# Performance work log

Measured on AMD Instinct MI355X. Metric: run time of the kernel, lower is better.

## Reference

```python
import jax, jax.numpy as jnp
import numpy as np

N, E, B = 25000, 400000, 64
IN, HID, OUT, EDGE, TDIM, L = 16, 128, 16, 16, 64, 4
EIN = 2 * HID + 1 + EDGE  # 273


def _sinusoidal(t, dim):
    half = dim // 2
    freqs = jnp.exp(jnp.arange(half, dtype=jnp.float32) * (-np.log(10000.0) / (half - 1)))
    a = t[:, None] * freqs[None, :]
    return jnp.concatenate([jnp.sin(a), jnp.cos(a)], axis=-1)


def _layernorm(h, g, b, eps=1e-5):
    mu = h.mean(-1, keepdims=True)
    v = h.var(-1, keepdims=True)
    return (h - mu) / jnp.sqrt(v + eps) * g + b


def setup_inputs() -> dict:
    key = jax.random.key(0)
    ks = iter(jax.random.split(key, 64))

    def rn(shape, scale=0.05):
        return jax.random.normal(next(ks), shape, dtype=jnp.float32) * scale

    inp = {
        'h': jax.random.normal(next(ks), (N, IN), dtype=jnp.float32),
        'x': jax.random.normal(next(ks), (N, 3), dtype=jnp.float32),
        'edge_index': jax.random.randint(next(ks), (2, E), 0, N),
        't': jax.random.uniform(next(ks), (B,), dtype=jnp.float32) * 1000.0,
        'edge_attr': jax.random.normal(next(ks), (E, EDGE), dtype=jnp.float32),
        'batch': jnp.sort(jax.random.randint(next(ks), (N,), 0, B)),
        # embeddings
        'node_w': rn((IN, HID)), 'node_b': jnp.zeros((HID,), jnp.float32),
        'tw1': rn((TDIM, HID)), 'tb1': jnp.zeros((HID,), jnp.float32),
        'tw2': rn((HID, HID)), 'tb2': jnp.zeros((HID,), jnp.float32),
        # per-layer stacked params (L, ...)
        'edge_w1': rn((L, EIN, HID)), 'edge_b1': jnp.zeros((L, HID), jnp.float32),
        'edge_w2': rn((L, HID, HID)), 'edge_b2': jnp.zeros((L, HID), jnp.float32),
        'att_w': rn((L, HID, 1)), 'att_b': jnp.zeros((L, 1), jnp.float32),
        'cw1': rn((L, HID, HID)), 'cb1': jnp.zeros((L, HID), jnp.float32),
        'cw2': rn((L, HID, 1), scale=0.001),  # xavier gain=0.001
        'nw1': rn((L, 2 * HID, HID)), 'nb1': jnp.zeros((L, HID), jnp.float32),
        'nw2': rn((L, HID, HID)), 'nb2': jnp.zeros((L, HID), jnp.float32),
        'ln_g': jnp.ones((L, HID), jnp.float32), 'ln_b': jnp.zeros((L, HID), jnp.float32),
        # heads
        'out_w1': rn((HID, HID)), 'out_b1': jnp.zeros((HID,), jnp.float32),
        'out_w2': rn((HID, OUT)), 'out_b2': jnp.zeros((OUT,), jnp.float32),
        'head_w': rn((HID, 3), scale=0.01), 'head_b': jnp.zeros((3,), jnp.float32),
    }
    return inp


def reference(h, x, edge_index, t, edge_attr, batch,
              node_w, node_b, tw1, tb1, tw2, tb2,
              edge_w1, edge_b1, edge_w2, edge_b2, att_w, att_b,
              cw1, cb1, cw2, nw1, nb1, nw2, nb2, ln_g, ln_b,
              out_w1, out_b1, out_w2, out_b2, head_w, head_b):
    silu = jax.nn.silu
    n_nodes = h.shape[0]
    row, col = edge_index[0], edge_index[1]

    # node + time embedding
    h = h @ node_w + node_b
    te = _sinusoidal(t, TDIM)
    te = silu(te @ tw1 + tb1) @ tw2 + tb2
    h = h + te[batch]

    for i in range(L):
        coord_diff = x[row] - x[col]                      # (E, 3)
        radial = (coord_diff ** 2).sum(-1, keepdims=True)  # (E, 1)
        edge_in = jnp.concatenate([h[row], h[col], radial, edge_attr], axis=-1)
        m = silu(silu(edge_in @ edge_w1[i] + edge_b1[i]) @ edge_w2[i] + edge_b2[i])
        att = jax.nn.sigmoid(m @ att_w[i] + att_b[i])
        m = m * att
        cw = silu(m @ cw1[i] + cb1[i]) @ cw2[i]           # (E, 1)
        coord_diff = coord_diff / jnp.sqrt(radial + 1e-8)  # normalize=True
        x = x + jax.ops.segment_sum(coord_diff * cw, row, num_segments=n_nodes)
        m_i = jax.ops.segment_sum(m, row, num_segments=n_nodes)
        h_in = jnp.concatenate([h, m_i], axis=-1)
        h_new = h + (silu(h_in @ nw1[i] + nb1[i]) @ nw2[i] + nb2[i])
        h = _layernorm(h_new, ln_g[i], ln_b[i])

    h_out = silu(h @ out_w1 + out_b1) @ out_w2 + out_b2  # (N, OUT)
    x_out = h @ head_w + head_b                           # (N, 3)
    return h_out, x_out
```

## Files before the change

kernel.cpp:

```cpp
#include <hip/hip_runtime.h>
#include <hip/hip_bf16.h>
#include <cmath>

#define NN      25000
#define NEDGE   400000
#define NBATCH  64
#define IN_DIM  16
#define HID     128
#define OUT_DIM 16
#define EDGE_DIM 16
#define TDIM    64
#define NL      4
#define EIN     273
#define EPB     64
#define W2KB    16
#define A_PAD   65
#define A3OFF   (16*A_PAD*8)
#define NPB     32
#define NPAD    33

typedef short bfrag __attribute__((ext_vector_type(8)));
typedef float ffrag __attribute__((ext_vector_type(4)));

__device__ __forceinline__ float siluf(float v) { return v / (1.f + __expf(-v)); }
__device__ __forceinline__ float sigm(float v)  { return 1.f / (1.f + __expf(-v)); }
__device__ __forceinline__ unsigned short f2b(float f) {
    unsigned u = __float_as_uint(f);
    u = (u + 0x7FFFu + ((u >> 16) & 1u)) >> 16;
    return (unsigned short)u;
}
__device__ __forceinline__ float b2f(unsigned short b) {
    return __uint_as_float(((unsigned)b) << 16);
}
__device__ __forceinline__ int ileave(int n) {
    return (n & 0x60) | ((n & 15) << 1) | ((n >> 4) & 1);
}

__global__ __launch_bounds__(256) void hist_kernel(const int* __restrict__ row, int* __restrict__ deg) {
    const int tid = blockIdx.x * 256 + threadIdx.x;
    if (tid < NEDGE) atomicAdd(&deg[row[tid]], 1);
}

__global__ __launch_bounds__(1024) void scan_kernel(const int* __restrict__ deg, int* __restrict__ row_start) {
    __shared__ int part[1024];
    const int tid = threadIdx.x;
    const int base = tid * 25;
    int sum = 0;
    for (int i = 0; i < 25; i++) { const int idx = base + i; if (idx < NN) sum += deg[idx]; }
    part[tid] = sum;
    __syncthreads();
    for (int off = 1; off < 1024; off <<= 1) {
        int v = (tid >= off) ? part[tid - off] : 0;
        __syncthreads();
        part[tid] += v;
        __syncthreads();
    }
    int run = part[tid] - sum;
    for (int i = 0; i < 25; i++) {
        const int idx = base + i;
        if (idx < NN) { row_start[idx] = run; run += deg[idx]; }
    }
    if (tid == 1023) row_start[NN] = part[1023];
}

__global__ __launch_bounds__(256) void scatter_kernel(
    const int* __restrict__ row, const int* __restrict__ col,
    const int* __restrict__ row_start, int* __restrict__ cursor,
    int* __restrict__ rowp, int* __restrict__ colp, int* __restrict__ eorder)
{
    const int tid = blockIdx.x * 256 + threadIdx.x;
    if (tid >= NEDGE) return;
    const int r = row[tid];
    const int pos = row_start[r] + atomicAdd(&cursor[r], 1);
    rowp[pos] = r; colp[pos] = col[tid]; eorder[pos] = tid;
}

__global__ __launch_bounds__(256) void ea_pack(
    const float* __restrict__ ea, const int* __restrict__ eorder, unsigned short* __restrict__ eabp)
{
    const int tid = blockIdx.x * 256 + threadIdx.x;
    if (tid >= NEDGE) return;
    const int e = eorder[tid];
    const float4* src = (const float4*)&ea[(size_t)e * 16];
    bfrag o0, o1;
    #pragma unroll
    for (int q = 0; q < 2; q++) {
        const float4 a = src[q];
        o0[q*4+0] = (short)f2b(a.x); o0[q*4+1] = (short)f2b(a.y);
        o0[q*4+2] = (short)f2b(a.z); o0[q*4+3] = (short)f2b(a.w);
    }
    #pragma unroll
    for (int q = 0; q < 2; q++) {
        const float4 a = src[2+q];
        o1[q*4+0] = (short)f2b(a.x); o1[q*4+1] = (short)f2b(a.y);
        o1[q*4+2] = (short)f2b(a.z); o1[q*4+3] = (short)f2b(a.w);
    }
    *(bfrag*)&eabp[(size_t)tid * 16]     = o0;
    *(bfrag*)&eabp[(size_t)tid * 16 + 8] = o1;
}

__global__ __launch_bounds__(256) void prep_w(
    const float* __restrict__ ew1, const float* __restrict__ ew2, const float* __restrict__ cw1,
    unsigned short* __restrict__ w1x, unsigned short* __restrict__ w1rp,
    unsigned short* __restrict__ w1cp, unsigned short* __restrict__ w2p,
    unsigned short* __restrict__ c1p)
{
    const int PER_L = 68 * 128;
    int tid = blockIdx.x * 256 + threadIdx.x;
    if (tid >= NL * PER_L) return;
    const int l = tid / PER_L, rem = tid % PER_L;
    const int kb = rem >> 7, n = rem & 127;
    unsigned short o[8];
    const float* W1 = ew1 + (size_t)l * EIN * HID;
    if (kb < 4) {
        const int nc = ileave(n);
        #pragma unroll
        for (int j = 0; j < 8; j++) {
            const int kk = kb * 8 + j;
            const int ok = (kk < 16) ? (257 + kk) : (kk == 16 ? 256 : -1);
            o[j] = (ok >= 0) ? f2b(W1[(size_t)ok * HID + nc]) : (unsigned short)0;
        }
        #pragma unroll
        for (int j = 0; j < 8; j++) w1x[(((size_t)l * 4 + kb) * 128 + n) * 8 + j] = o[j];
    } else if (kb < 20) {
        const int kb2 = kb - 4;
        const int nc = ileave(n);
        #pragma unroll
        for (int j = 0; j < 8; j++) o[j] = f2b(W1[(size_t)(kb2 * 8 + j) * HID + nc]);
        #pragma unroll
        for (int j = 0; j < 8; j++) w1rp[(((size_t)l * 16 + kb2) * 128 + n) * 8 + j] = o[j];
    } else if (kb < 36) {
        const int kb2 = kb - 20;
        const int nc = ileave(n);
        #pragma unroll
        for (int j = 0; j < 8; j++) o[j] = f2b(W1[(size_t)(128 + kb2 * 8 + j) * HID + nc]);
        #pragma unroll
        for (int j = 0; j < 8; j++) w1cp[(((size_t)l * 16 + kb2) * 128 + n) * 8 + j] = o[j];
    } else if (kb < 52) {
        const int kb2 = kb - 36;
        const float* W = ew2 + (size_t)l * HID * HID;
        const int nc = ileave(n);
        #pragma unroll
        for (int j = 0; j < 8; j++) o[j] = f2b(W[(size_t)(kb2 * 8 + j) * HID + nc]);
        #pragma unroll
        for (int j = 0; j < 8; j++) w2p[(((size_t)l * W2KB + kb2) * 128 + n) * 8 + j] = o[j];
    } else {
        const int kb2 = kb - 52;
        const float* W = cw1 + (size_t)l * HID * HID;
        #pragma unroll
        for (int j = 0; j < 8; j++) o[j] = f2b(W[(size_t)(kb2 * 8 + j) * HID + n]);
        #pragma unroll
        for (int j = 0; j < 8; j++) c1p[(((size_t)l * W2KB + kb2) * 128 + n) * 8 + j] = o[j];
    }
}

__global__ __launch_bounds__(256) void prep_w2(
    const float* __restrict__ nw1, const float* __restrict__ nw2,
    const float* __restrict__ ow1, const float* __restrict__ ow2,
    unsigned short* __restrict__ n1p, unsigned short* __restrict__ n2p,
    unsigned short* __restrict__ o1p, unsigned short* __restrict__ o2p)
{
    const int C1 = NL * 32 * 128;
    const int C2 = C1 + NL * 16 * 128;
    const int C3 = C2 + 16 * 128;
    const int C4 = C3 + 16 * 16;
    int tid = blockIdx.x * 256 + threadIdx.x;
    if (tid >= C4) return;
    if (tid < C1) {
        const int l = tid / (32*128), rem = tid % (32*128);
        const int kb = rem >> 7, n = rem & 127;
        const int nc = ileave(n);
        #pragma unroll
        for (int j = 0; j < 8; j++)
            n1p[(size_t)tid*8 + j] = f2b(nw1[((size_t)l*256 + kb*8 + j)*128 + nc]);
    } else if (tid < C2) {
        const int t2 = tid - C1;
        const int l = t2 / (16*128), rem = t2 % (16*128);
        const int kb = rem >> 7, n = rem & 127;
        const int nc = ileave(n);
        #pragma unroll
        for (int j = 0; j < 8; j++)
            n2p[(size_t)t2*8 + j] = f2b(nw2[((size_t)l*128 + kb*8 + j)*128 + nc]);
    } else if (tid < C3) {
        const int t2 = tid - C2;
        const int kb = t2 >> 7, n = t2 & 127;
        #pragma unroll
        for (int j = 0; j < 8; j++)
            o1p[(size_t)t2*8 + j] = f2b(ow1[(size_t)(kb*8 + j)*128 + n]);
    } else {
        const int t2 = tid - C3;
        const int kb = t2 >> 4, n = t2 & 15;
        #pragma unroll
        for (int j = 0; j < 8; j++)
            o2p[(size_t)t2*8 + j] = f2b(ow2[(size_t)(kb*8 + j)*16 + n]);
    }
}

__global__ __launch_bounds__(HID) void te_kernel(
    const float* __restrict__ t, const float* __restrict__ tw1, const float* __restrict__ tb1,
    const float* __restrict__ tw2, const float* __restrict__ tb2, float* __restrict__ te_out)
{
    __shared__ float s0[TDIM];
    __shared__ float s1[HID];
    const int b = blockIdx.x, j = threadIdx.x;
    const float tv = t[b];
    if (j < TDIM) {
        const int k = j & 31;
        const float freq = expf((float)k * (-logf(10000.f) / 31.f));
        const float a = tv * freq;
        s0[j] = (j < 32) ? sinf(a) : cosf(a);
    }
    __syncthreads();
    float acc = tb1[j];
    for (int k = 0; k < TDIM; k++) acc += s0[k] * tw1[k*HID + j];
    s1[j] = siluf(acc);
    __syncthreads();
    float acc2 = tb2[j];
    for (int k = 0; k < HID; k++) acc2 += s1[k] * tw2[k*HID + j];
    te_out[b*HID + j] = acc2;
}

__global__ __launch_bounds__(256) void embed_kernel(
    const float* __restrict__ h_in, const float* __restrict__ x_in,
    const int* __restrict__ batch,
    const float* __restrict__ node_w, const float* __restrict__ node_b,
    const float* __restrict__ te, float* __restrict__ h, unsigned short* __restrict__ hbf,
    float* __restrict__ x0, float* __restrict__ m_i)
{
    __shared__ float hs[2][IN_DIM];
    const int local = threadIdx.x >> 7;
    const int j = threadIdx.x & 127;
    const int n = blockIdx.x * 2 + local;
    if (j < IN_DIM) hs[local][j] = h_in[n*IN_DIM + j];
    if (j >= 64 && j < 67) x0[n*3 + (j - 64)] = x_in[n*3 + (j - 64)];
    __syncthreads();
    float acc = node_b[j];
    #pragma unroll
    for (int k = 0; k < IN_DIM; k++) acc += hs[local][k] * node_w[k*HID + j];
    acc += te[batch[n]*HID + j];
    h[(size_t)n*HID + j]   = acc;
    hbf[(size_t)n*HID + j] = f2b(acc);
    m_i[(size_t)n*HID + j] = 0.f;
}

__global__ __launch_bounds__(256) void pq_kernel(
    const unsigned short* __restrict__ hbf,
    const unsigned short* __restrict__ Wr, const unsigned short* __restrict__ Wc,
    unsigned short* __restrict__ P, unsigned short* __restrict__ Q)
{
    __shared__ unsigned short sA[16 * A_PAD * 8];
    const int t = threadIdx.x, lane = t & 63, w = t >> 6;
    const int quad = lane >> 4, colid = lane & 15;
    const int n0 = blockIdx.x * 64;

    #pragma unroll
    for (int it = 0; it < 4; it++) {
        const int c = t + it * 256;
        const int e = c >> 4, kb = c & 15;
        const int nidx = min(n0 + e, NN - 1);
        *(bfrag*)&sA[(kb*A_PAD + e) * 8] = *(const bfrag*)&hbf[(size_t)nidx * HID + kb * 8];
    }
    __syncthreads();

    ffrag aP[4][2] = {}, aQ[4][2] = {};
    for (int ks = 0; ks < 4; ks++) {
        const int kb = ks * 4 + quad;
        const bfrag p0 = *(const bfrag*)&Wr[((size_t)kb * 128 + w*32 + colid) * 8];
        const bfrag p1 = *(const bfrag*)&Wr[((size_t)kb * 128 + w*32 + 16 + colid) * 8];
        const bfrag q0 = *(const bfrag*)&Wc[((size_t)kb * 128 + w*32 + colid) * 8];
        const bfrag q1 = *(const bfrag*)&Wc[((size_t)kb * 128 + w*32 + 16 + colid) * 8];
        #pragma unroll
        for (int mt = 0; mt < 4; mt++) {
            const bfrag a = *(const bfrag*)&sA[(kb*A_PAD + mt*16 + colid) * 8];
            aP[mt][0] = __builtin_amdgcn_mfma_f32_16x16x32_bf16(a, p0, aP[mt][0], 0, 0, 0);
            aP[mt][1] = __builtin_amdgcn_mfma_f32_16x16x32_bf16(a, p1, aP[mt][1], 0, 0, 0);
            aQ[mt][0] = __builtin_amdgcn_mfma_f32_16x16x32_bf16(a, q0, aQ[mt][0], 0, 0, 0);
            aQ[mt][1] = __builtin_amdgcn_mfma_f32_16x16x32_bf16(a, q1, aQ[mt][1], 0, 0, 0);
        }
    }
    const int f0 = w*32 + 2*colid;
    #pragma unroll
    for (int mt = 0; mt < 4; mt++)
        #pragma unroll
        for (int reg = 0; reg < 4; reg++) {
            const int n = n0 + mt*16 + quad*4 + reg;
            if (n < NN) {
                *(__hip_bfloat162*)&P[(size_t)n*HID + f0] =
                    __float22bfloat162_rn(make_float2(aP[mt][0][reg], aP[mt][1][reg]));
                *(__hip_bfloat162*)&Q[(size_t)n*HID + f0] =
                    __float22bfloat162_rn(make_float2(aQ[mt][0][reg], aQ[mt][1][reg]));
            }
        }
}

__global__ __launch_bounds__(256) void edge_mfma(
    const unsigned short* __restrict__ P, const unsigned short* __restrict__ Q,
    const float* __restrict__ x,
    float* __restrict__ x_new, float* __restrict__ m_i,
    const int* __restrict__ rowp, const int* __restrict__ colp,
    const unsigned short* __restrict__ eabp,
    const unsigned short* __restrict__ W1X, const float* __restrict__ B1,
    const unsigned short* __restrict__ W2p, const float* __restrict__ B2,
    const unsigned short* __restrict__ C1p, const float* __restrict__ CB1,
    const float* __restrict__ AW, const float* __restrict__ ABv,
    const float* __restrict__ CW2)
{
    __shared__ unsigned short sA[32 * A_PAD * 8];
    __shared__ int rc[EPB][2];
    __shared__ float AWs[HID];
    float* scr   = (float*)sA;
    float* attS  = scr;
    float* cpart = scr + 64;

    const int t = threadIdx.x;
    const int e0 = blockIdx.x * EPB;
    const int lane = t & 63, w = t >> 6;
    const int quad = lane >> 4, colid = lane & 15;
    const int f0 = w*32 + 2*colid;

    float cd0 = 0.f, cd1 = 0.f, cd2 = 0.f;
    if (t < EPB) {
        const int r = rowp[e0 + t], c = colp[e0 + t];
        rc[t][0] = r; rc[t][1] = c;
        const float dx = x[r*3+0] - x[c*3+0];
        const float dy = x[r*3+1] - x[c*3+1];
        const float dz = x[r*3+2] - x[c*3+2];
        const float rad = dx*dx + dy*dy + dz*dz;
        const float inv = 1.f / sqrtf(rad + 1e-8f);
        cd0 = dx*inv; cd1 = dy*inv; cd2 = dz*inv;
        unsigned short* p2 = &sA[A3OFF + (2*A_PAD + t) * 8];
        p2[0] = f2b(rad);
        #pragma unroll
        for (int j = 1; j < 8; j++) p2[j] = 0;
        unsigned short* p3 = &sA[A3OFF + (3*A_PAD + t) * 8];
        #pragma unroll
        for (int j = 0; j < 8; j++) p3[j] = 0;
    }
    if (t >= 128 && t < 256) AWs[t - 128] = AW[t - 128];
    if (t < 128) {
        const int e = t >> 1, hh = t & 1;
        *(bfrag*)&sA[A3OFF + (hh*A_PAD + e) * 8] = *(const bfrag*)&eabp[(size_t)(e0 + e) * 16 + hh * 8];
    }
    __syncthreads();

    ffrag accea[4][2];
    {
        const float b0v = B1[f0], b1v = B1[f0+1];
        #pragma unroll
        for (int mt = 0; mt < 4; mt++)
            #pragma unroll
            for (int r = 0; r < 4; r++) { accea[mt][0][r] = b0v; accea[mt][1][r] = b1v; }
    }
    {
        const bfrag eb0 = *(const bfrag*)&W1X[((size_t)quad * 128 + w*32 + colid) * 8];
        const bfrag eb1 = *(const bfrag*)&W1X[((size_t)quad * 128 + w*32 + 16 + colid) * 8];
        #pragma unroll
        for (int mt = 0; mt < 4; mt++) {
            const bfrag a = *(const bfrag*)&sA[A3OFF + (quad*A_PAD + mt*16 + colid) * 8];
            accea[mt][0] = __builtin_amdgcn_mfma_f32_16x16x32_bf16(a, eb0, accea[mt][0], 0, 0, 0);
            accea[mt][1] = __builtin_amdgcn_mfma_f32_16x16x32_bf16(a, eb1, accea[mt][1], 0, 0, 0);
        }
    }

    {
        const int kb = f0 >> 3, j = f0 & 7;
        #pragma unroll
        for (int mt = 0; mt < 4; mt++) {
            unsigned pv[4], qv[4];
            #pragma unroll
            for (int reg = 0; reg < 4; reg++) {
                const int e = mt*16 + quad*4 + reg;
                pv[reg] = *(const unsigned*)&P[(size_t)rc[e][0]*HID + f0];
                qv[reg] = *(const unsigned*)&Q[(size_t)rc[e][1]*HID + f0];
            }
            #pragma unroll
            for (int reg = 0; reg < 4; reg++) {
                const int e = mt*16 + quad*4 + reg;
                const float v0 = siluf(__uint_as_float(pv[reg] << 16)
                                     + __uint_as_float(qv[reg] << 16) + accea[mt][0][reg]);
                const float v1 = siluf(__uint_as_float(pv[reg] & 0xFFFF0000u)
                                     + __uint_as_float(qv[reg] & 0xFFFF0000u) + accea[mt][1][reg]);
                *(__hip_bfloat162*)&sA[(kb*A_PAD + e) * 8 + j] =
                    __float22bfloat162_rn(make_float2(v0, v1));
            }
        }
    }
    __syncthreads();

    ffrag acc2[4][2] = {};
    for (int ks = 0; ks < 4; ks++) {
        const int kb = ks * 4 + quad;
        const bfrag b0 = *(const bfrag*)&W2p[((size_t)kb * 128 + w*32 + colid) * 8];
        const bfrag b1 = *(const bfrag*)&W2p[((size_t)kb * 128 + w*32 + 16 + colid) * 8];
        #pragma unroll
        for (int mt = 0; mt < 4; mt++) {
            const bfrag a = *(const bfrag*)&sA[(kb*A_PAD + mt*16 + colid) * 8];
            acc2[mt][0] = __builtin_amdgcn_mfma_f32_16x16x32_bf16(a, b0, acc2[mt][0], 0, 0, 0);
            acc2[mt][1] = __builtin_amdgcn_mfma_f32_16x16x32_bf16(a, b1, acc2[mt][1], 0, 0, 0);
        }
    }
    {
        const int kb = f0 >> 3, j = f0 & 7;
        const float b0v = B2[f0], b1v = B2[f0+1];
        #pragma unroll
        for (int mt = 0; mt < 4; mt++)
            #pragma unroll
            for (int reg = 0; reg < 4; reg++) {
                const float v0 = siluf(acc2[mt][0][reg] + b0v);
                const float v1 = siluf(acc2[mt][1][reg] + b1v);
                const int e = mt*16 + quad*4 + reg;
                *(__hip_bfloat162*)&sA[A3OFF + (kb*A_PAD + e) * 8 + j] =
                    __float22bfloat162_rn(make_float2(v0, v1));
            }
    }
    __syncthreads();

    {
        const int e = t >> 2, q = t & 3;
        float s = 0.f;
        #pragma unroll
        for (int kk = 0; kk < 4; kk++) {
            const int kb = q*4 + kk;
            const bfrag v = *(const bfrag*)&sA[A3OFF + (kb*A_PAD + e) * 8];
            #pragma unroll
            for (int j = 0; j < 8; j++) s += b2f((unsigned short)v[j]) * AWs[kb*8 + j];
        }
        s += __shfl_xor(s, 1);
        s += __shfl_xor(s, 2);
        if (q == 0) attS[e] = sigm(s + ABv[0]);
    }
    __syncthreads();

    ffrag acc3[4][2] = {};
    for (int ks = 0; ks < 4; ks++) {
        const int kb = ks * 4 + quad;
        const bfrag b0 = *(const bfrag*)&C1p[((size_t)kb * 128 + w*32 + colid) * 8];
        const bfrag b1 = *(const bfrag*)&C1p[((size_t)kb * 128 + w*32 + 16 + colid) * 8];
        #pragma unroll
        for (int mt = 0; mt < 4; mt++) {
            const bfrag a = *(const bfrag*)&sA[A3OFF + (kb*A_PAD + mt*16 + colid) * 8];
            acc3[mt][0] = __builtin_amdgcn_mfma_f32_16x16x32_bf16(a, b0, acc3[mt][0], 0, 0, 0);
            acc3[mt][1] = __builtin_amdgcn_mfma_f32_16x16x32_bf16(a, b1, acc3[mt][1], 0, 0, 0);
        }
    }

    {
        const int fkb0 = lane >> 3,     fj = lane & 7;
        const int fkb1 = 8 + (lane >> 3);
        float a0 = 0.f, a1 = 0.f;
        for (int i = 0; i < 16; i++) {
            const int e = (w << 4) + i;
            const float av = attS[e];
            const int r = rc[e][0];
            a0 += b2f(sA[A3OFF + (fkb0*A_PAD + e) * 8 + fj]) * av;
            a1 += b2f(sA[A3OFF + (fkb1*A_PAD + e) * 8 + fj]) * av;
            const bool flush = (i == 15) || (rc[e+1][0] != r);
            if (flush) {
                atomicAdd(&m_i[(size_t)r * HID + lane],      a0);
                atomicAdd(&m_i[(size_t)r * HID + lane + 64], a1);
                a0 = 0.f; a1 = 0.f;
            }
        }
    }

    {
        const float cb0v = CB1[w*32 + colid], cb1v = CB1[w*32 + 16 + colid];
        const float cwv0 = CW2[w*32 + colid], cwv1 = CW2[w*32 + 16 + colid];
        float att_r[4][4];
        #pragma unroll
        for (int mt = 0; mt < 4; mt++) {
            const float4 a4 = *(const float4*)&attS[mt*16 + quad*4];
            att_r[mt][0] = a4.x; att_r[mt][1] = a4.y; att_r[mt][2] = a4.z; att_r[mt][3] = a4.w;
        }
        float p[4][4];
        #pragma unroll
        for (int mt = 0; mt < 4; mt++)
            #pragma unroll
            for (int reg = 0; reg < 4; reg++)
                p[mt][reg] = siluf(att_r[mt][reg] * acc3[mt][0][reg] + cb0v) * cwv0
                           + siluf(att_r[mt][reg] * acc3[mt][1][reg] + cb1v) * cwv1;
        __syncthreads();
        #pragma unroll
        for (int mt = 0; mt < 4; mt++)
            #pragma unroll
            for (int reg = 0; reg < 4; reg++) {
                float s = p[mt][reg];
                s += __shfl_xor(s, 1);
                s += __shfl_xor(s, 2);
                s += __shfl_xor(s, 4);
                s += __shfl_xor(s, 8);
                if (colid == 0) cpart[(mt*16 + quad*4 + reg) * 4 + w] = s;
            }
    }
    __syncthreads();
    if (t < EPB) {
        const float s = cpart[t*4+0] + cpart[t*4+1] + cpart[t*4+2] + cpart[t*4+3];
        const int r = rc[t][0];
        atomicAdd(&x_new[r*3+0], cd0 * s);
        atomicAdd(&x_new[r*3+1], cd1 * s);
        atomicAdd(&x_new[r*3+2], cd2 * s);
    }
}

__global__ __launch_bounds__(256) void node_mfma(
    float* __restrict__ h, unsigned short* __restrict__ hbf, float* __restrict__ m_i,
    const unsigned short* __restrict__ N1p, const float* __restrict__ NB1,
    const unsigned short* __restrict__ N2p, const float* __restrict__ NB2,
    const float* __restrict__ LG, const float* __restrict__ LB)
{
    __shared__ unsigned short sA[32 * NPAD * 8];
    __shared__ float mu_s[NPB], rs_s[NPB];
    float* hres = (float*)sA;

    const int t = threadIdx.x, lane = t & 63, w = t >> 6;
    const int quad = lane >> 4, colid = lane & 15;
    const int n0 = blockIdx.x * NPB;

    #pragma unroll
    for (int it = 0; it < 2; it++) {
        const int c = t + it * 256;
        const int e = c >> 4, kb = c & 15;
        const int nidx = min(n0 + e, NN - 1);
        *(bfrag*)&sA[(kb*NPAD + e) * 8] = *(const bfrag*)&hbf[(size_t)nidx * HID + kb * 8];
    }
    #pragma unroll
    for (int it = 0; it < 2; it++) {
        const int c = t + it * 256;
        const int e = c >> 4, kb = c & 15;
        const int nidx = min(n0 + e, NN - 1);
        const float4 v0 = *(const float4*)&m_i[(size_t)nidx * HID + kb * 8];
        const float4 v1 = *(const float4*)&m_i[(size_t)nidx * HID + kb * 8 + 4];
        bfrag bv;
        bv[0]=(short)f2b(v0.x); bv[1]=(short)f2b(v0.y); bv[2]=(short)f2b(v0.z); bv[3]=(short)f2b(v0.w);
        bv[4]=(short)f2b(v1.x); bv[5]=(short)f2b(v1.y); bv[6]=(short)f2b(v1.z); bv[7]=(short)f2b(v1.w);
        *(bfrag*)&sA[((16 + kb)*NPAD + e) * 8] = bv;
        if (n0 + e < NN) {
            const float4 z4 = {0.f, 0.f, 0.f, 0.f};
            *(float4*)&m_i[(size_t)nidx * HID + kb * 8]     = z4;
            *(float4*)&m_i[(size_t)nidx * HID + kb * 8 + 4] = z4;
        }
    }
    __syncthreads();

    const int f0 = w*32 + 2*colid;
    ffrag acc1[2][2];
    {
        const float b0v = NB1[f0], b1v = NB1[f0+1];
        #pragma unroll
        for (int mt = 0; mt < 2; mt++)
            #pragma unroll
            for (int r = 0; r < 4; r++) { acc1[mt][0][r] = b0v; acc1[mt][1][r] = b1v; }
    }
    for (int ks = 0; ks < 8; ks++) {
        const int kb = ks * 4 + quad;
        const bfrag b0 = *(const bfrag*)&N1p[((size_t)kb * 128 + w*32 + colid) * 8];
        const bfrag b1 = *(const bfrag*)&N1p[((size_t)kb * 128 + w*32 + 16 + colid) * 8];
        #pragma unroll
        for (int mt = 0; mt < 2; mt++) {
            const bfrag a = *(const bfrag*)&sA[(kb*NPAD + mt*16 + colid) * 8];
            acc1[mt][0] = __builtin_amdgcn_mfma_f32_16x16x32_bf16(a, b0, acc1[mt][0], 0, 0, 0);
            acc1[mt][1] = __builtin_amdgcn_mfma_f32_16x16x32_bf16(a, b1, acc1[mt][1], 0, 0, 0);
        }
    }
    __syncthreads();
    {
        const int kb = f0 >> 3, j = f0 & 7;
        #pragma unroll
        for (int mt = 0; mt < 2; mt++)
            #pragma unroll
            for (int reg = 0; reg < 4; reg++) {
                const float v0 = siluf(acc1[mt][0][reg]);
                const float v1 = siluf(acc1[mt][1][reg]);
                const int e = mt*16 + quad*4 + reg;
                *(__hip_bfloat162*)&sA[(kb*NPAD + e) * 8 + j] =
                    __float22bfloat162_rn(make_float2(v0, v1));
            }
    }
    __syncthreads();

    ffrag acc2[2][2];
    {
        const float b0v = NB2[f0], b1v = NB2[f0+1];
        #pragma unroll
        for (int mt = 0; mt < 2; mt++)
            #pragma unroll
            for (int r = 0; r < 4; r++) { acc2[mt][0][r] = b0v; acc2[mt][1][r] = b1v; }
    }
    for (int ks = 0; ks < 4; ks++) {
        const int kb = ks * 4 + quad;
        const bfrag b0 = *(const bfrag*)&N2p[((size_t)kb * 128 + w*32 + colid) * 8];
        const bfrag b1 = *(const bfrag*)&N2p[((size_t)kb * 128 + w*32 + 16 + colid) * 8];
        #pragma unroll
        for (int mt = 0; mt < 2; mt++) {
            const bfrag a = *(const bfrag*)&sA[(kb*NPAD + mt*16 + colid) * 8];
            acc2[mt][0] = __builtin_amdgcn_mfma_f32_16x16x32_bf16(a, b0, acc2[mt][0], 0, 0, 0);
            acc2[mt][1] = __builtin_amdgcn_mfma_f32_16x16x32_bf16(a, b1, acc2[mt][1], 0, 0, 0);
        }
    }
    __syncthreads();
    {
        #pragma unroll
        for (int mt = 0; mt < 2; mt++)
            #pragma unroll
            for (int reg = 0; reg < 4; reg++) {
                const int row = mt*16 + quad*4 + reg;
                const int nidx = min(n0 + row, NN - 1);
                const float2 hr = *(const float2*)&h[(size_t)nidx*HID + f0];
                float2 o;
                o.x = acc2[mt][0][reg] + hr.x;
                o.y = acc2[mt][1][reg] + hr.y;
                *(float2*)&hres[row*130 + f0] = o;
            }
    }
    __syncthreads();
    {
        const int row = t >> 3, q = t & 7;
        float s = 0.f, s2 = 0.f;
        #pragma unroll
        for (int i = 0; i < 16; i++) {
            const float v = hres[row*130 + q*16 + i];
            s += v; s2 += v*v;
        }
        s += __shfl_xor(s, 1); s2 += __shfl_xor(s2, 1);
        s += __shfl_xor(s, 2); s2 += __shfl_xor(s2, 2);
        s += __shfl_xor(s, 4); s2 += __shfl_xor(s2, 4);
        if (q == 0) {
            const float mu = s * (1.f/HID);
            mu_s[row] = mu;
            rs_s[row] = rsqrtf(s2 * (1.f/HID) - mu*mu + 1e-5f);
        }
    }
    __syncthreads();
    for (int idx = t; idx < NPB*HID; idx += 256) {
        const int row = idx >> 7, f = idx & 127;
        const int n = n0 + row;
        if (n < NN) {
            const float v = (hres[row*130 + f] - mu_s[row]) * rs_s[row] * LG[f] + LB[f];
            h[(size_t)n*HID + f]   = v;
            hbf[(size_t)n*HID + f] = f2b(v);
        }
    }
}

__global__ __launch_bounds__(256) void out_mfma(
    const unsigned short* __restrict__ hbf,
    const unsigned short* __restrict__ O1p, const float* __restrict__ OB1,
    const unsigned short* __restrict__ O2p, const float* __restrict__ OB2,
    const float* __restrict__ HW, const float* __restrict__ HB,
    float* __restrict__ out)
{
    __shared__ unsigned short sA[32 * A_PAD * 8];
    __shared__ float hws[HID*3];
    const int A2O = 16 * A_PAD * 8;

    const int t = threadIdx.x, lane = t & 63, w = t >> 6;
    const int quad = lane >> 4, colid = lane & 15;
    const int n0 = blockIdx.x * 64;

    if (t < 128)      { hws[t] = HW[t]; hws[t+128] = HW[t+128]; }
    else if (t < 256) { const int i = t - 128 + 256; if (i < 384) hws[i] = HW[i]; }
    #pragma unroll
    for (int it = 0; it < 4; it++) {
        const int c = t + it * 256;
        const int e = c >> 4, kb = c & 15;
        const int nidx = min(n0 + e, NN - 1);
        *(bfrag*)&sA[(kb*A_PAD + e) * 8] = *(const bfrag*)&hbf[(size_t)nidx * HID + kb * 8];
    }
    __syncthreads();

    ffrag acc1[4][2];
    {
        const float b0v = OB1[w*32 + colid], b1v = OB1[w*32 + 16 + colid];
        #pragma unroll
        for (int mt = 0; mt < 4; mt++)
            #pragma unroll
            for (int r = 0; r < 4; r++) { acc1[mt][0][r] = b0v; acc1[mt][1][r] = b1v; }
    }
    for (int ks = 0; ks < 4; ks++) {
        const int kb = ks * 4 + quad;
        const bfrag b0 = *(const bfrag*)&O1p[((size_t)kb * 128 + w*32 + colid) * 8];
        const bfrag b1 = *(const bfrag*)&O1p[((size_t)kb * 128 + w*32 + 16 + colid) * 8];
        #pragma unroll
        for (int mt = 0; mt < 4; mt++) {
            const bfrag a = *(const bfrag*)&sA[(kb*A_PAD + mt*16 + colid) * 8];
            acc1[mt][0] = __builtin_amdgcn_mfma_f32_16x16x32_bf16(a, b0, acc1[mt][0], 0, 0, 0);
            acc1[mt][1] = __builtin_amdgcn_mfma_f32_16x16x32_bf16(a, b1, acc1[mt][1], 0, 0, 0);
        }
    }
    {
        #pragma unroll
        for (int mt = 0; mt < 4; mt++)
            #pragma unroll
            for (int nt = 0; nt < 2; nt++) {
                const int f = w*32 + nt*16 + colid;
                const int kb = f >> 3, j = f & 7;
                #pragma unroll
                for (int reg = 0; reg < 4; reg++) {
                    const float v = siluf(acc1[mt][nt][reg]);
                    const int e = mt*16 + quad*4 + reg;
                    sA[A2O + (kb*A_PAD + e) * 8 + j] = f2b(v);
                }
            }
    }
    __syncthreads();

    ffrag acco;
    {
        const float ob2v = OB2[colid];
        #pragma unroll
        for (int r = 0; r < 4; r++) acco[r] = ob2v;
    }
    for (int ks = 0; ks < 4; ks++) {
        const int kb = ks * 4 + quad;
        const bfrag a = *(const bfrag*)&sA[A2O + (kb*A_PAD + w*16 + colid) * 8];
        const bfrag b = *(const bfrag*)&O2p[((size_t)kb * 16 + colid) * 8];
        acco = __builtin_amdgcn_mfma_f32_16x16x32_bf16(a, b, acco, 0, 0, 0);
    }
    #pragma unroll
    for (int reg = 0; reg < 4; reg++) {
        const int rowg = w*16 + quad*4 + reg;
        const int n = n0 + rowg;
        if (n < NN) out[(size_t)n*OUT_DIM + colid] = acco[reg];
    }

    {
        const int rloc = t >> 2, q = t & 3;
        float s0 = 0.f, s1 = 0.f, s2 = 0.f;
        #pragma unroll
        for (int kk = 0; kk < 4; kk++) {
            const int kb = q*4 + kk;
            const bfrag v = *(const bfrag*)&sA[(kb*A_PAD + rloc) * 8];
            #pragma unroll
            for (int j = 0; j < 8; j++) {
                const float hv = b2f((unsigned short)v[j]);
                const int k = kb*8 + j;
                s0 += hv * hws[k*3+0]; s1 += hv * hws[k*3+1]; s2 += hv * hws[k*3+2];
            }
        }
        s0 += __shfl_xor(s0, 1); s1 += __shfl_xor(s1, 1); s2 += __shfl_xor(s2, 1);
        s0 += __shfl_xor(s0, 2); s1 += __shfl_xor(s1, 2); s2 += __shfl_xor(s2, 2);
        const int n = n0 + rloc;
        if (q == 0 && n < NN) {
            out[(size_t)NN*OUT_DIM + n*3 + 0] = s0 + HB[0];
            out[(size_t)NN*OUT_DIM + n*3 + 1] = s1 + HB[1];
            out[(size_t)NN*OUT_DIM + n*3 + 2] = s2 + HB[2];
        }
    }
}

extern "C" void kernel_launch(void* const* d_in, const int* in_sizes, int n_in,
                              void* d_out, int out_size, void* d_ws, size_t ws_size,
                              hipStream_t stream) {
    (void)in_sizes; (void)n_in; (void)out_size; (void)ws_size;
    const float* h_in      = (const float*)d_in[0];
    const float* x_in      = (const float*)d_in[1];
    const int*   edge_idx  = (const int*)  d_in[2];
    const float* t         = (const float*)d_in[3];
    const float* edge_attr = (const float*)d_in[4];
    const int*   batch     = (const int*)  d_in[5];
    const float* node_w = (const float*)d_in[6];
    const float* node_b = (const float*)d_in[7];
    const float* tw1    = (const float*)d_in[8];
    const float* tb1    = (const float*)d_in[9];
    const float* tw2    = (const float*)d_in[10];
    const float* tb2    = (const float*)d_in[11];
    const float* ew1    = (const float*)d_in[12];
    const float* eb1    = (const float*)d_in[13];
    const float* ew2    = (const float*)d_in[14];
    const float* eb2    = (const float*)d_in[15];
    const float* attw   = (const float*)d_in[16];
    const float* attb   = (const float*)d_in[17];
    const float* cw1    = (const float*)d_in[18];
    const float* cb1    = (const float*)d_in[19];
    const float* cw2    = (const float*)d_in[20];
    const float* nw1    = (const float*)d_in[21];
    const float* nb1    = (const float*)d_in[22];
    const float* nw2    = (const float*)d_in[23];
    const float* nb2    = (const float*)d_in[24];
    const float* lng    = (const float*)d_in[25];
    const float* lnb    = (const float*)d_in[26];
    const float* ow1    = (const float*)d_in[27];
    const float* ob1    = (const float*)d_in[28];
    const float* ow2    = (const float*)d_in[29];
    const float* ob2    = (const float*)d_in[30];
    const float* hw     = (const float*)d_in[31];
    const float* hb     = (const float*)d_in[32];

    const int* row = edge_idx;
    const int* col = edge_idx + NEDGE;

    float* ws  = (float*)d_ws;
    float* te  = ws;
    float* h   = te  + NBATCH*HID;
    float* m_i = h   + (size_t)NN*HID;
    float* x0  = m_i + (size_t)NN*HID;
    float* x1  = x0  + NN*3;
    unsigned short* hbf  = (unsigned short*)(x1 + NN*3);
    unsigned short* eabp = hbf + (size_t)NN*HID;
    unsigned short* w1x  = eabp + (size_t)NEDGE*EDGE_DIM;
    unsigned short* w1rp = w1x  + (size_t)NL*4*128*8;
    unsigned short* w1cp = w1rp + (size_t)NL*16*128*8;
    unsigned short* w2p  = w1cp + (size_t)NL*16*128*8;
    unsigned short* c1p  = w2p  + (size_t)NL*16*128*8;
    unsigned short* n1p  = c1p  + (size_t)NL*16*128*8;
    unsigned short* n2p  = n1p  + (size_t)NL*32*128*8;
    unsigned short* o1p  = n2p  + (size_t)NL*16*128*8;
    unsigned short* o2p  = o1p  + (size_t)16*128*8;
    unsigned short* Pq   = o2p  + (size_t)16*16*8;
    unsigned short* Qq   = Pq   + (size_t)NN*HID;
    int* deg       = (int*)(Qq + (size_t)NN*HID);
    int* row_start = deg + NN;
    int* cursor    = row_start + NN + 1;
    int* rowp      = cursor + NN;
    int* colp      = rowp + NEDGE;
    int* eorder    = colp + NEDGE;

    hipMemsetAsync(deg, 0, NN*sizeof(int), stream);
    hipMemsetAsync(cursor, 0, NN*sizeof(int), stream);
    hist_kernel<<<(NEDGE+255)/256, 256, 0, stream>>>(row, deg);
    scan_kernel<<<1, 1024, 0, stream>>>(deg, row_start);
    scatter_kernel<<<(NEDGE+255)/256, 256, 0, stream>>>(row, col, row_start, cursor, rowp, colp, eorder);
    ea_pack<<<(NEDGE+255)/256, 256, 0, stream>>>(edge_attr, eorder, eabp);

    prep_w<<<(NL*68*128 + 255)/256, 256, 0, stream>>>(ew1, ew2, cw1, w1x, w1rp, w1cp, w2p, c1p);
    prep_w2<<<(NL*32*128 + NL*16*128 + 16*128 + 16*16 + 255)/256, 256, 0, stream>>>(
        nw1, nw2, ow1, ow2, n1p, n2p, o1p, o2p);
    te_kernel<<<NBATCH, HID, 0, stream>>>(t, tw1, tb1, tw2, tb2, te);
    embed_kernel<<<NN/2, 256, 0, stream>>>(h_in, x_in, batch, node_w, node_b, te, h, hbf, x0, m_i);

    const int NBLK = (NN + NPB - 1) / NPB;
    const int OBLK = (NN + 63) / 64;
    float* xc = x0; float* xn = x1;
    for (int i = 0; i < NL; i++) {
        pq_kernel<<<OBLK, 256, 0, stream>>>(
            hbf, w1rp + (size_t)i*16*128*8, w1cp + (size_t)i*16*128*8, Pq, Qq);
        hipMemcpyAsync(xn, xc, (size_t)NN*3*sizeof(float), hipMemcpyDeviceToDevice, stream);
        edge_mfma<<<NEDGE/EPB, 256, 0, stream>>>(
            Pq, Qq, xc, xn, m_i, rowp, colp, eabp,
            w1x + (size_t)i*4*128*8, eb1 + (size_t)i*HID,
            w2p + (size_t)i*16*128*8, eb2 + (size_t)i*HID,
            c1p + (size_t)i*16*128*8, cb1 + (size_t)i*HID,
            attw + (size_t)i*HID, attb + i,
            cw2 + (size_t)i*HID);
        node_mfma<<<NBLK, 256, 0, stream>>>(
            h, hbf, m_i,
            n1p + (size_t)i*32*128*8, nb1 + (size_t)i*HID,
            n2p + (size_t)i*16*128*8, nb2 + (size_t)i*HID,
            lng + (size_t)i*HID,      lnb + (size_t)i*HID);
        float* tmp = xc; xc = xn; xn = tmp;
    }

    out_mfma<<<OBLK, 256, 0, stream>>>(hbf, o1p, ob1, o2p, ob2, hw, hb, (float*)d_out);
}
```

Measured before the change: 1.077 ms.

## Store P/Q in fp32, use rcp in silu, replace shuffle reduction with LDS

The per-node P and Q projections are now stored as fp32 instead of bf16, so the edge kernel gathers float2 values and drops the bf16 unpacking, at the cost of twice the gather bytes. silu and sigmoid use the hardware reciprocal instead of a division. The coordinate-weight reduction no longer runs a four-step cross-lane shuffle per edge; partials go into an LDS scratch buffer and 64 threads each sum 64 values serially.

```diff
diff --git a/kernel.cpp b/kernel.cpp
--- a/kernel.cpp
+++ b/kernel.cpp
@@ -22,8 +22,8 @@
 typedef short bfrag __attribute__((ext_vector_type(8)));
 typedef float ffrag __attribute__((ext_vector_type(4)));
 
-__device__ __forceinline__ float siluf(float v) { return v / (1.f + __expf(-v)); }
-__device__ __forceinline__ float sigm(float v)  { return 1.f / (1.f + __expf(-v)); }
+__device__ __forceinline__ float siluf(float v) { return v * __builtin_amdgcn_rcpf(1.f + __expf(-v)); }
+__device__ __forceinline__ float sigm(float v)  { return __builtin_amdgcn_rcpf(1.f + __expf(-v)); }
 __device__ __forceinline__ unsigned short f2b(float f) {
     unsigned u = __float_as_uint(f);
     u = (u + 0x7FFFu + ((u >> 16) & 1u)) >> 16;
@@ -246,7 +246,7 @@
 __global__ __launch_bounds__(256) void pq_kernel(
     const unsigned short* __restrict__ hbf,
     const unsigned short* __restrict__ Wr, const unsigned short* __restrict__ Wc,
-    unsigned short* __restrict__ P, unsigned short* __restrict__ Q)
+    float* __restrict__ P, float* __restrict__ Q)
 {
     __shared__ unsigned short sA[16 * A_PAD * 8];
     const int t = threadIdx.x, lane = t & 63, w = t >> 6;
@@ -285,16 +285,14 @@
         for (int reg = 0; reg < 4; reg++) {
             const int n = n0 + mt*16 + quad*4 + reg;
             if (n < NN) {
-                *(__hip_bfloat162*)&P[(size_t)n*HID + f0] =
-                    __float22bfloat162_rn(make_float2(aP[mt][0][reg], aP[mt][1][reg]));
-                *(__hip_bfloat162*)&Q[(size_t)n*HID + f0] =
-                    __float22bfloat162_rn(make_float2(aQ[mt][0][reg], aQ[mt][1][reg]));
+                *(float2*)&P[(size_t)n*HID + f0] = make_float2(aP[mt][0][reg], aP[mt][1][reg]);
+                *(float2*)&Q[(size_t)n*HID + f0] = make_float2(aQ[mt][0][reg], aQ[mt][1][reg]);
             }
         }
 }
 
 __global__ __launch_bounds__(256) void edge_mfma(
-    const unsigned short* __restrict__ P, const unsigned short* __restrict__ Q,
+    const float* __restrict__ P, const float* __restrict__ Q,
     const float* __restrict__ x,
     float* __restrict__ x_new, float* __restrict__ m_i,
     const int* __restrict__ rowp, const int* __restrict__ colp,
@@ -308,9 +306,9 @@
     __shared__ unsigned short sA[32 * A_PAD * 8];
     __shared__ int rc[EPB][2];
     __shared__ float AWs[HID];
-    float* scr   = (float*)sA;
-    float* attS  = scr;
-    float* cpart = scr + 64;
+    float* scr  = (float*)sA;
+    float* attS = scr;
+    float* pscr = scr;
 
     const int t = threadIdx.x;
     const int e0 = blockIdx.x * EPB;
@@ -366,20 +364,18 @@
         const int kb = f0 >> 3, j = f0 & 7;
         #pragma unroll
         for (int mt = 0; mt < 4; mt++) {
-            unsigned pv[4], qv[4];
+            float2 pv[4], qv[4];
             #pragma unroll
             for (int reg = 0; reg < 4; reg++) {
                 const int e = mt*16 + quad*4 + reg;
-                pv[reg] = *(const unsigned*)&P[(size_t)rc[e][0]*HID + f0];
-                qv[reg] = *(const unsigned*)&Q[(size_t)rc[e][1]*HID + f0];
+                pv[reg] = *(const float2*)&P[(size_t)rc[e][0]*HID + f0];
+                qv[reg] = *(const float2*)&Q[(size_t)rc[e][1]*HID + f0];
             }
             #pragma unroll
             for (int reg = 0; reg < 4; reg++) {
                 const int e = mt*16 + quad*4 + reg;
-                const float v0 = siluf(__uint_as_float(pv[reg] << 16)
-                                     + __uint_as_float(qv[reg] << 16) + accea[mt][0][reg]);
-                const float v1 = siluf(__uint_as_float(pv[reg] & 0xFFFF0000u)
-                                     + __uint_as_float(qv[reg] & 0xFFFF0000u) + accea[mt][1][reg]);
+                const float v0 = siluf(pv[reg].x + qv[reg].x + accea[mt][0][reg]);
+                const float v1 = siluf(pv[reg].y + qv[reg].y + accea[mt][1][reg]);
                 *(__hip_bfloat162*)&sA[(kb*A_PAD + e) * 8 + j] =
                     __float22bfloat162_rn(make_float2(v0, v1));
             }
@@ -463,38 +459,36 @@
         }
     }
 
+    float p[4][4];
     {
         const float cb0v = CB1[w*32 + colid], cb1v = CB1[w*32 + 16 + colid];
         const float cwv0 = CW2[w*32 + colid], cwv1 = CW2[w*32 + 16 + colid];
-        float att_r[4][4];
         #pragma unroll
         for (int mt = 0; mt < 4; mt++) {
             const float4 a4 = *(const float4*)&attS[mt*16 + quad*4];
-            att_r[mt][0] = a4.x; att_r[mt][1] = a4.y; att_r[mt][2] = a4.z; att_r[mt][3] = a4.w;
-        }
-        float p[4][4];
+            const float att_r[4] = {a4.x, a4.y, a4.z, a4.w};
+            #pragma unroll
+            for (int reg = 0; reg < 4; reg++)
+                p[mt][reg] = siluf(att_r[reg] * acc3[mt][0][reg] + cb0v) * cwv0
+                           + siluf(att_r[reg] * acc3[mt][1][reg] + cb1v) * cwv1;
+        }
+    }
+    __syncthreads();
+    {
+        const int k = w*16 + colid;
         #pragma unroll
         for (int mt = 0; mt < 4; mt++)
             #pragma unroll
-            for (int reg = 0; reg < 4; reg++)
-                p[mt][reg] = siluf(att_r[mt][reg] * acc3[mt][0][reg] + cb0v) * cwv0
-                           + siluf(att_r[mt][reg] * acc3[mt][1][reg] + cb1v) * cwv1;
-        __syncthreads();
-        #pragma unroll
-        for (int mt = 0; mt < 4; mt++)
-            #pragma unroll
-            for (int reg = 0; reg < 4; reg++) {
-                float s = p[mt][reg];
-                s += __shfl_xor(s, 1);
-                s += __shfl_xor(s, 2);
-                s += __shfl_xor(s, 4);
-                s += __shfl_xor(s, 8);
-                if (colid == 0) cpart[(mt*16 + quad*4 + reg) * 4 + w] = s;
+            for (int rr = 0; rr < 2; rr++) {
+                const int e = mt*16 + quad*4 + rr*2;
+                *(float2*)&pscr[k*66 + e] = make_float2(p[mt][rr*2], p[mt][rr*2+1]);
             }
     }
     __syncthreads();
     if (t < EPB) {
-        const float s = cpart[t*4+0] + cpart[t*4+1] + cpart[t*4+2] + cpart[t*4+3];
+        float s = 0.f;
+        #pragma unroll
+        for (int k2 = 0; k2 < 64; k2++) s += pscr[k2*66 + t];
         const int r = rc[t][0];
         atomicAdd(&x_new[r*3+0], cd0 * s);
         atomicAdd(&x_new[r*3+1], cd1 * s);
@@ -795,7 +789,9 @@
     float* m_i = h   + (size_t)NN*HID;
     float* x0  = m_i + (size_t)NN*HID;
     float* x1  = x0  + NN*3;
-    unsigned short* hbf  = (unsigned short*)(x1 + NN*3);
+    float* Pq  = x1  + NN*3;
+    float* Qq  = Pq  + (size_t)NN*HID;
+    unsigned short* hbf  = (unsigned short*)(Qq + (size_t)NN*HID);
     unsigned short* eabp = hbf + (size_t)NN*HID;
     unsigned short* w1x  = eabp + (size_t)NEDGE*EDGE_DIM;
     unsigned short* w1rp = w1x  + (size_t)NL*4*128*8;
@@ -806,9 +802,7 @@
     unsigned short* n2p  = n1p  + (size_t)NL*32*128*8;
     unsigned short* o1p  = n2p  + (size_t)NL*16*128*8;
     unsigned short* o2p  = o1p  + (size_t)16*128*8;
-    unsigned short* Pq   = o2p  + (size_t)16*16*8;
-    unsigned short* Qq   = Pq   + (size_t)NN*HID;
-    int* deg       = (int*)(Qq + (size_t)NN*HID);
+    int* deg       = (int*)(o2p + (size_t)16*16*8);
     int* row_start = deg + NN;
     int* cursor    = row_start + NN + 1;
     int* rowp      = cursor + NN;
```

Result: no change. 1.082 ms (+0.4%).
